# Kernel optimization log

Hardware: AMD Instinct MI355X
Metric: run time of the kernel (lower is better)

Reference implementation:

```python
import jax, jax.numpy as jnp
import numpy as np

H, D, K, FF = 4, 256, 1024, 1024  # n_head, d_model, key_feature_dim, dim_feedforward
L, B = 2048, 4                    # pixels, batch


def setup_inputs() -> dict:
    key = jax.random.key(0)
    ks = jax.random.split(key, 12)
    def g(k, shape, s=0.02):
        return jax.random.normal(k, shape, jnp.float32) * s
    return dict(
        src=jax.random.normal(ks[0], (L, B, D), jnp.float32),
        WK=g(ks[1], (H, K, D), (2.0 / K) ** 0.5),
        WQ=g(ks[2], (H, K, D), (2.0 / K) ** 0.5),
        WV=g(ks[3], (H, D, D), (2.0 / D) ** 0.5),
        TC=g(ks[4], (H, D, D)),
        ENw1=g(ks[5], (H, FF, D)), ENb1=jnp.zeros((H, FF), jnp.float32),
        ENw2=g(ks[6], (H, D, FF)), ENb2=jnp.zeros((H, D), jnp.float32),
        ENg=jnp.ones((H, D), jnp.float32), ENbeta=jnp.zeros((H, D), jnp.float32),
        Wout=g(ks[7], (D, H * D)),
        L1w=g(ks[8], (FF, D)), L1b=jnp.zeros((FF,), jnp.float32),
        L2w=g(ks[9], (D, FF)), L2b=jnp.zeros((D,), jnp.float32),
        N1g=jnp.ones((D,), jnp.float32), N1b=jnp.zeros((D,), jnp.float32),
        N2g=jnp.ones((D,), jnp.float32), N2b=jnp.zeros((D,), jnp.float32),
    )


def _ln(x, g, b, eps=1e-5):
    m = jnp.mean(x, -1, keepdims=True)
    v = jnp.mean((x - m) ** 2, -1, keepdims=True)
    return (x - m) * jax.lax.rsqrt(v + eps) * g + b


def _l2n(x, eps=1e-12):
    n = jnp.sqrt(jnp.sum(x * x, -1, keepdims=True))
    return x / jnp.maximum(n, eps)


def reference(src, WK, WQ, WV, TC, ENw1, ENb1, ENw2, ENb2, ENg, ENbeta,
              Wout, L1w, L1b, L2w, L2b, N1g, N1b, N2g, N2b):
    # --- RMA: per-head RelationUnit, vectorized over head axis h ---
    wq = _l2n(jnp.einsum('lbd,hkd->hlbk', src, WQ))   # (H,L,B,K), L2-normed
    wk = _l2n(jnp.einsum('lbd,hkd->hlbk', src, WK))
    wv = jnp.einsum('lbd,hed->hlbe', src, WV)         # (H,L,B,D)
    dot = jnp.einsum('hlbk,hmbk->hblm', wq, wk)       # (H,B,Lq,Lk)
    aff = jax.nn.softmax(dot, axis=-1)                 # softmax over keys (temp=1)
    aff = aff / (1e-9 + jnp.sum(aff, axis=2, keepdims=True))  # renorm over QUERY dim (torch dim=1)
    out = jnp.einsum('hblm,hmbe->hlbe', aff, wv)       # (H,L,B,D)
    ru = jax.nn.relu(jnp.einsum('hlbe,hfe->hlbf', src[None] - out, TC))
    # per-head extra TransNonlinear: residual MLP + layernorm
    hid = jax.nn.relu(jnp.einsum('hlbd,hfd->hlbf', ru, ENw1) + ENb1[:, None, None, :])
    s2 = jnp.einsum('hlbf,hdf->hlbd', hid, ENw2) + ENb2[:, None, None, :]
    tn = _ln(ru + s2, ENg[:, None, None, :], ENbeta[:, None, None, :])  # (H,L,B,D)
    concat = jnp.transpose(tn, (1, 2, 0, 3)).reshape(L, B, H * D)
    attn = concat @ Wout.T                              # (L,B,D)
    # --- encoder layer: residual + LN + FFN + LN (dropout = eval identity) ---
    x = _ln(src + attn, N1g, N1b)
    ff = jax.nn.relu(x @ L1w.T + L1b) @ L2w.T + L2b
    return _ln(x + ff, N2g, N2b)
```

## Files before the change

### kernel.cpp

```cpp
#include <hip/hip_runtime.h>
#include <hip/hip_bf16.h>

typedef __hip_bfloat16 bf16;
typedef short s16x8 __attribute__((ext_vector_type(8)));
typedef float f32x4 __attribute__((ext_vector_type(4)));

#define HN 4
#define DM 256
#define KF 1024
#define FFD 1024
#define LL 2048
#define BB 4
#define NN (LL * BB)
#define HD (HN * DM)

__device__ __forceinline__ float b2f(unsigned short u) {
    unsigned v = ((unsigned)u) << 16; float f; __builtin_memcpy(&f, &v, 4); return f;
}
__device__ __forceinline__ unsigned short f2b(float f) {
    bf16 b = (bf16)f; unsigned short u; __builtin_memcpy(&u, &b, 2); return u;
}

__device__ __forceinline__ float waveReduceSum(float v) {
    for (int o = 32; o; o >>= 1) v += __shfl_down(v, o, 64);
    return v;
}
__device__ __forceinline__ float waveReduceMax(float v) {
    for (int o = 32; o; o >>= 1) v = fmaxf(v, __shfl_down(v, o, 64));
    return v;
}
__device__ __forceinline__ float blockReduceSum(float v) {
    __shared__ float sh[4];
    v = waveReduceSum(v);
    __syncthreads();
    if ((threadIdx.x & 63) == 0) sh[threadIdx.x >> 6] = v;
    __syncthreads();
    return sh[0] + sh[1] + sh[2] + sh[3];
}
__device__ __forceinline__ float blockReduceMax(float v) {
    __shared__ float sh[4];
    v = waveReduceMax(v);
    __syncthreads();
    if ((threadIdx.x & 63) == 0) sh[threadIdx.x >> 6] = v;
    __syncthreads();
    return fmaxf(fmaxf(sh[0], sh[1]), fmaxf(sh[2], sh[3]));
}

__global__ void sentinel_kernel(float* out, float val) {
    if (threadIdx.x == 0 && blockIdx.x == 0) out[0] = val;
}

__device__ __forceinline__ void gll16(const void* g, void* l) {
#if defined(__HIP_DEVICE_COMPILE__)
    __builtin_amdgcn_global_load_lds(
        (const __attribute__((address_space(1))) unsigned int*)g,
        (__attribute__((address_space(3))) unsigned int*)l, 16, 0, 0);
#endif
}

#define VMC(n) asm volatile("s_waitcnt vmcnt(" #n ")" ::: "memory")
#define LGKM0() asm volatile("s_waitcnt lgkmcnt(0)" ::: "memory")

__global__ __launch_bounds__(512) void gemm256(
    const bf16* __restrict__ A, int lda, long sA,
    const bf16* __restrict__ Bv, int ldb, long sB,
    void* __restrict__ C, int cF32, int ldc, long sC,
    int Kc,
    const float* __restrict__ bias, long sBias,
    const void* __restrict__ aux, int auxType, int ldaux, long sAux,
    float accSign, int relu)
{
    const int z = blockIdx.z;
    const bf16* Ah = A + (long)z * sA;
    const bf16* Bh = Bv + (long)z * sB;
    float* Cf = (float*)C + (long)z * sC;
    bf16*  Ch = (bf16*)C + (long)z * sC;
    const float* biasp = bias ? (bias + (long)z * sBias) : nullptr;
    const float* auxf = (auxType == 1) ? ((const float*)aux + (long)z * sAux) : nullptr;
    const bf16*  auxh = (auxType == 2) ? ((const bf16*)aux + (long)z * sAux) : nullptr;

    __shared__ __align__(16) bf16 As[2][256 * 64];
    __shared__ __align__(16) bf16 Bs[2][256 * 64];

    const int tid  = threadIdx.x;
    const int lane = tid & 63;
    const int wid  = __builtin_amdgcn_readfirstlane(tid >> 6);
    const int wm   = wid >> 2;
    const int wn   = wid & 3;
    const int lrow = lane & 15;
    const int quad = lane >> 4;
    const int m0 = blockIdx.x * 256;
    const int n0 = blockIdx.y * 256;

    const int srow8  = wid * 8 + (lane >> 3);
    const int scolsw = ((lane & 7) * 8) ^ ((srow8 & 7) << 3);
    const bf16* Aorg = Ah + (long)m0 * lda;
    const bf16* Borg = Bh + (long)n0 * ldb;

    const int colx = (lane & 7) << 3;
    const int kc0 = (quad * 8) ^ colx;
    const int kc1 = (32 + quad * 8) ^ colx;

    f32x4 acc[8][4] = {};
    s16x8 afr[4][2], bfr[4][2];

    const int nk = Kc >> 6;

    auto stg = [&](const bf16* org, int ld, bf16* lds, int k0, int h) {
#pragma unroll
        for (int j = 0; j < 2; j++) {
            int rl = h * 128 + j * 64 + srow8;
            gll16((const void*)(org + (long)rl * ld + k0 + scolsw),
                  (void*)(lds + (h * 128 + j * 64 + wid * 8) * 64));
        }
    };

    stg(Aorg, lda, As[0], 0, 0); stg(Aorg, lda, As[0], 0, 1);
    stg(Borg, ldb, Bs[0], 0, 0); stg(Borg, ldb, Bs[0], 0, 1);
    if (nk > 1) {
        stg(Aorg, lda, As[1], 64, 0); stg(Aorg, lda, As[1], 64, 1);
        stg(Borg, ldb, Bs[1], 64, 0); stg(Borg, ldb, Bs[1], 64, 1);
        VMC(8);
    } else {
        VMC(0);
    }
    __builtin_amdgcn_s_barrier();

    for (int t = 0; t < nk; ++t) {
        const int s = t & 1;
        const bf16* Acur = As[s];
        const bf16* Bcur = Bs[s];
        bf16* Anxt = As[s ^ 1];
        bf16* Bslot = Bs[s];
        const bool stA = (t >= 1) && (t + 1 < nk);
        const bool stB = (t + 2 < nk);

#pragma unroll
        for (int mi = 0; mi < 4; mi++) {
            int r = (wm * 128 + mi * 16 + lrow) * 64;
            afr[mi][0] = *(const s16x8*)&Acur[r + kc0];
            afr[mi][1] = *(const s16x8*)&Acur[r + kc1];
        }
#pragma unroll
        for (int ni = 0; ni < 2; ni++) {
            int r = (wn * 64 + ni * 16 + lrow) * 64;
            bfr[ni][0] = *(const s16x8*)&Bcur[r + kc0];
            bfr[ni][1] = *(const s16x8*)&Bcur[r + kc1];
        }
        if (stA) stg(Aorg, lda, Anxt, (t + 1) << 6, 0);
        __builtin_amdgcn_s_barrier();
        LGKM0();
        __builtin_amdgcn_s_setprio(1);
#pragma unroll
        for (int mi = 0; mi < 4; mi++)
#pragma unroll
            for (int ni = 0; ni < 2; ni++)
#pragma unroll
                for (int ks = 0; ks < 2; ks++)
                    acc[mi][ni] = __builtin_amdgcn_mfma_f32_16x16x32_bf16(afr[mi][ks], bfr[ni][ks], acc[mi][ni], 0, 0, 0);
        __builtin_amdgcn_s_setprio(0);
        __builtin_amdgcn_s_barrier();

#pragma unroll
        for (int ni = 0; ni < 2; ni++) {
            int r = (wn * 64 + (2 + ni) * 16 + lrow) * 64;
            bfr[2 + ni][0] = *(const s16x8*)&Bcur[r + kc0];
            bfr[2 + ni][1] = *(const s16x8*)&Bcur[r + kc1];
        }
        if (stA) stg(Aorg, lda, Anxt, (t + 1) << 6, 1);
        __builtin_amdgcn_s_barrier();
        LGKM0();
        __builtin_amdgcn_s_setprio(1);
#pragma unroll
        for (int mi = 0; mi < 4; mi++)
#pragma unroll
            for (int ni = 0; ni < 2; ni++)
#pragma unroll
                for (int ks = 0; ks < 2; ks++)
                    acc[mi][2 + ni] = __builtin_amdgcn_mfma_f32_16x16x32_bf16(afr[mi][ks], bfr[2 + ni][ks], acc[mi][2 + ni], 0, 0, 0);
        __builtin_amdgcn_s_setprio(0);
        __builtin_amdgcn_s_barrier();

#pragma unroll
        for (int mi = 0; mi < 4; mi++) {
            int r = (wm * 128 + 64 + mi * 16 + lrow) * 64;
            afr[mi][0] = *(const s16x8*)&Acur[r + kc0];
            afr[mi][1] = *(const s16x8*)&Acur[r + kc1];
        }
        if (stB) stg(Borg, ldb, Bslot, (t + 2) << 6, 0);
        __builtin_amdgcn_s_barrier();
        LGKM0();
        __builtin_amdgcn_s_setprio(1);
#pragma unroll
        for (int mi = 0; mi < 4; mi++)
#pragma unroll
            for (int ni = 0; ni < 2; ni++)
#pragma unroll
                for (int ks = 0; ks < 2; ks++)
                    acc[4 + mi][ni] = __builtin_amdgcn_mfma_f32_16x16x32_bf16(afr[mi][ks], bfr[ni][ks], acc[4 + mi][ni], 0, 0, 0);
        __builtin_amdgcn_s_setprio(0);
        __builtin_amdgcn_s_barrier();

        if (stB) stg(Borg, ldb, Bslot, (t + 2) << 6, 1);
        __builtin_amdgcn_s_barrier();
        __builtin_amdgcn_s_setprio(1);
#pragma unroll
        for (int mi = 0; mi < 4; mi++)
#pragma unroll
            for (int ni = 0; ni < 2; ni++)
#pragma unroll
                for (int ks = 0; ks < 2; ks++)
                    acc[4 + mi][2 + ni] = __builtin_amdgcn_mfma_f32_16x16x32_bf16(afr[mi][ks], bfr[2 + ni][ks], acc[4 + mi][2 + ni], 0, 0, 0);
        __builtin_amdgcn_s_setprio(0);
        if (stB) { VMC(4); } else { VMC(0); }
        __builtin_amdgcn_s_barrier();
    }

#pragma unroll
    for (int mi = 0; mi < 8; mi++) {
#pragma unroll
        for (int ni = 0; ni < 4; ni++) {
            int col = n0 + wn * 64 + ni * 16 + lrow;
            float bvl = biasp ? biasp[col] : 0.0f;
#pragma unroll
            for (int i = 0; i < 4; i++) {
                int row = m0 + wm * 128 + mi * 16 + quad * 4 + i;
                float v = accSign * acc[mi][ni][i] + bvl;
                if (auxType == 1) v += auxf[(long)row * ldaux + col];
                else if (auxType == 2) v += (float)auxh[(long)row * ldaux + col];
                if (relu) v = fmaxf(v, 0.0f);
                if (cF32) Cf[(long)row * ldc + col] = v;
                else Ch[(long)row * ldc + col] = (bf16)v;
            }
        }
    }
}

template<int BN>
__global__ __launch_bounds__(256) void gemm_nt(
    const void* __restrict__ A, int aF32, int lda, long sA,
    const void* __restrict__ Bv, int bF32, int ldb, long sB,
    void* __restrict__ C, int cF32, int ldc, long sC,
    int Kc,
    const float* __restrict__ bias, long sBias,
    const void* __restrict__ aux, int auxType, int ldaux, long sAux,
    float accSign, int relu)
{
    constexpr int NI = BN / 32;
    constexpr int WN = BN / 2;
    const int z = blockIdx.z;
    const float* Af = (const float*)A + (long)z * sA;
    const bf16*  Ah = (const bf16*)A + (long)z * sA;
    const float* Bf = (const float*)Bv + (long)z * sB;
    const bf16*  Bh = (const bf16*)Bv + (long)z * sB;
    float* Cf = (float*)C + (long)z * sC;
    bf16*  Ch = (bf16*)C + (long)z * sC;
    const float* biasp = bias ? (bias + (long)z * sBias) : nullptr;
    const float* auxf = (auxType == 1) ? ((const float*)aux + (long)z * sAux) : nullptr;
    const bf16*  auxh = (auxType == 2) ? ((const bf16*)aux + (long)z * sAux) : nullptr;

    __shared__ __align__(16) bf16 As[2][128 * 32];
    __shared__ __align__(16) bf16 Bs[2][BN * 32];

    const int tid = threadIdx.x;
    const int lane = tid & 63;
    const int wv = __builtin_amdgcn_readfirstlane(tid >> 6);
    const int wm = (tid >> 6) & 1;
    const int wn = (tid >> 6) >> 1;
    const int lrow = lane & 15;
    const int quad = lane >> 4;
    const int m0 = blockIdx.x * 128;
    const int n0 = blockIdx.y * BN;
    const int srow = tid >> 1;
    const int scol = (tid & 1) * 16;
    const int drow = wv * 16 + (lane >> 2);
    const int dcol = (lane & 3) * 8;

    f32x4 acc[4][NI] = {};

    if (!aF32 && !bF32) {
        const int nk = Kc >> 5;
        auto stage = [&](int k0, int buf) {
            const bf16* a0 = Ah + (long)(m0 + drow) * lda + k0 + dcol;
            gll16((const void*)a0, (void*)&As[buf][wv * 512]);
            gll16((const void*)(a0 + (long)lda * 64), (void*)&As[buf][2048 + wv * 512]);
            const bf16* b0 = Bh + (long)(n0 + drow) * ldb + k0 + dcol;
            gll16((const void*)b0, (void*)&Bs[buf][wv * 512]);
            if (BN == 128)
                gll16((const void*)(b0 + (long)ldb * 64), (void*)&Bs[buf][2048 + wv * 512]);
        };
        stage(0, 0);
        __syncthreads();
        int cur = 0;
        for (int t = 0; t < nk; ++t) {
            if (t + 1 < nk) stage((t + 1) << 5, cur ^ 1);
            s16x8 af[4], bfg[NI];
#pragma unroll
            for (int mi = 0; mi < 4; mi++)
                af[mi] = *(const s16x8*)&As[cur][(wm * 64 + mi * 16 + lrow) * 32 + quad * 8];
#pragma unroll
            for (int ni = 0; ni < NI; ni++)
                bfg[ni] = *(const s16x8*)&Bs[cur][(wn * WN + ni * 16 + lrow) * 32 + quad * 8];
#pragma unroll
            for (int mi = 0; mi < 4; mi++)
#pragma unroll
                for (int ni = 0; ni < NI; ni++)
                    acc[mi][ni] = __builtin_amdgcn_mfma_f32_16x16x32_bf16(af[mi], bfg[ni], acc[mi][ni], 0, 0, 0);
            __syncthreads();
            cur ^= 1;
        }
    } else {
        for (int k0 = 0; k0 < Kc; k0 += 32) {
            uint4 av0, av1, bv0, bv1;
            if (aF32) {
                const float* ag = Af + (long)(m0 + srow) * lda + k0 + scol;
                ushort t[16];
#pragma unroll
                for (int j = 0; j < 4; j++) {
                    float4 f = *(const float4*)(ag + 4 * j);
                    t[4*j] = f2b(f.x); t[4*j+1] = f2b(f.y); t[4*j+2] = f2b(f.z); t[4*j+3] = f2b(f.w);
                }
                av0 = *(const uint4*)&t[0]; av1 = *(const uint4*)&t[8];
            }
            if (bF32) {
                if (srow < BN) {
                    const float* bg = Bf + (long)(n0 + srow) * ldb + k0 + scol;
                    ushort t[16];
#pragma unroll
                    for (int j = 0; j < 4; j++) {
                        float4 f = *(const float4*)(bg + 4 * j);
                        t[4*j] = f2b(f.x); t[4*j+1] = f2b(f.y); t[4*j+2] = f2b(f.z); t[4*j+3] = f2b(f.w);
                    }
                    bv0 = *(const uint4*)&t[0]; bv1 = *(const uint4*)&t[8];
                }
            }
            __syncthreads();
            if (aF32) {
                *(uint4*)&As[0][srow * 32 + scol] = av0;
                *(uint4*)&As[0][srow * 32 + scol + 8] = av1;
            } else {
                gll16((const void*)(Ah + (long)(m0 + drow) * lda + k0 + dcol), (void*)&As[0][wv * 512]);
                gll16((const void*)(Ah + (long)(m0 + 64 + drow) * lda + k0 + dcol), (void*)&As[0][2048 + wv * 512]);
            }
            if (bF32) {
                if (srow < BN) {
                    *(uint4*)&Bs[0][srow * 32 + scol] = bv0;
                    *(uint4*)&Bs[0][srow * 32 + scol + 8] = bv1;
                }
            } else {
                gll16((const void*)(Bh + (long)(n0 + drow) * ldb + k0 + dcol), (void*)&Bs[0][wv * 512]);
                if (BN == 128)
                    gll16((const void*)(Bh + (long)(n0 + 64 + drow) * ldb + k0 + dcol), (void*)&Bs[0][2048 + wv * 512]);
            }
            __syncthreads();

            s16x8 af[4], bfg[NI];
#pragma unroll
            for (int mi = 0; mi < 4; mi++)
                af[mi] = *(const s16x8*)&As[0][(wm * 64 + mi * 16 + lrow) * 32 + quad * 8];
#pragma unroll
            for (int ni = 0; ni < NI; ni++)
                bfg[ni] = *(const s16x8*)&Bs[0][(wn * WN + ni * 16 + lrow) * 32 + quad * 8];
#pragma unroll
            for (int mi = 0; mi < 4; mi++)
#pragma unroll
                for (int ni = 0; ni < NI; ni++)
                    acc[mi][ni] = __builtin_amdgcn_mfma_f32_16x16x32_bf16(af[mi], bfg[ni], acc[mi][ni], 0, 0, 0);
        }
    }

#pragma unroll
    for (int mi = 0; mi < 4; mi++) {
#pragma unroll
        for (int ni = 0; ni < NI; ni++) {
            int col = n0 + wn * WN + ni * 16 + lrow;
            float bvl = biasp ? biasp[col] : 0.0f;
#pragma unroll
            for (int i = 0; i < 4; i++) {
                int row = m0 + wm * 64 + mi * 16 + quad * 4 + i;
                float v = accSign * acc[mi][ni][i] + bvl;
                if (auxType == 1) v += auxf[(long)row * ldaux + col];
                else if (auxType == 2) v += (float)auxh[(long)row * ldaux + col];
                if (relu) v = fmaxf(v, 0.0f);
                if (cF32) Cf[(long)row * ldc + col] = v;
                else Ch[(long)row * ldc + col] = (bf16)v;
            }
        }
    }
}

__global__ __launch_bounds__(256) void cvt4(const float* __restrict__ in, bf16* __restrict__ out, int n4) {
    int i = blockIdx.x * 256 + threadIdx.x;
    if (i < n4) {
        float4 f = ((const float4*)in)[i];
        ushort4 u; u.x = f2b(f.x); u.y = f2b(f.y); u.z = f2b(f.z); u.w = f2b(f.w);
        ((ushort4*)out)[i] = u;
    }
}

struct WCvt {
    const float* in[9];
    bf16* out[9];
    int n4[9];
};
__global__ __launch_bounds__(256) void cvt_weights(WCvt wc) {
    int t = blockIdx.y;
    int n4 = wc.n4[t];
    const float4* in = (const float4*)wc.in[t];
    ushort4* out = (ushort4*)wc.out[t];
    for (int i = blockIdx.x * 256 + threadIdx.x; i < n4; i += gridDim.x * 256) {
        float4 f = in[i];
        ushort4 u; u.x = f2b(f.x); u.y = f2b(f.y); u.z = f2b(f.z); u.w = f2b(f.w);
        out[i] = u;
    }
}

__global__ __launch_bounds__(256) void l2norm_rows(bf16* __restrict__ Q) {
    bf16* q = Q + (long)blockIdx.x * KF;
    ushort4 u = ((ushort4*)q)[threadIdx.x];
    float v0 = b2f(u.x), v1 = b2f(u.y), v2 = b2f(u.z), v3 = b2f(u.w);
    float ss = blockReduceSum(v0 * v0 + v1 * v1 + v2 * v2 + v3 * v3);
    float inv = 1.0f / fmaxf(sqrtf(ss), 1e-12f);
    u.x = f2b(v0 * inv); u.y = f2b(v1 * inv); u.z = f2b(v2 * inv); u.w = f2b(v3 * inv);
    ((ushort4*)q)[threadIdx.x] = u;
}

__global__ __launch_bounds__(256) void softmax_rows(bf16* __restrict__ P) {
    bf16* p = P + (long)blockIdx.x * LL;
    ushort4 a = ((ushort4*)p)[2 * threadIdx.x];
    ushort4 b = ((ushort4*)p)[2 * threadIdx.x + 1];
    float v[8] = {b2f(a.x), b2f(a.y), b2f(a.z), b2f(a.w), b2f(b.x), b2f(b.y), b2f(b.z), b2f(b.w)};
    float mx = -1e30f;
#pragma unroll
    for (int i = 0; i < 8; i++) mx = fmaxf(mx, v[i]);
    mx = blockReduceMax(mx);
    float s = 0.0f;
#pragma unroll
    for (int i = 0; i < 8; i++) { v[i] = __expf(v[i] - mx); s += v[i]; }
    s = blockReduceSum(s);
    float inv = 1.0f / s;
    a.x = f2b(v[0]*inv); a.y = f2b(v[1]*inv); a.z = f2b(v[2]*inv); a.w = f2b(v[3]*inv);
    b.x = f2b(v[4]*inv); b.y = f2b(v[5]*inv); b.z = f2b(v[6]*inv); b.w = f2b(v[7]*inv);
    ((ushort4*)p)[2 * threadIdx.x] = a;
    ((ushort4*)p)[2 * threadIdx.x + 1] = b;
}

__global__ __launch_bounds__(256) void zero_cs(float* __restrict__ cs) {
    cs[blockIdx.x * 256 + threadIdx.x] = 0.0f;
}

__global__ __launch_bounds__(256) void colsum2(const bf16* __restrict__ P, float* __restrict__ cs) {
    int col = blockIdx.x * 256 + threadIdx.x;
    int rc = blockIdx.y;
    int b = blockIdx.z;
    const bf16* p = P + (long)b * LL * LL + (long)rc * 128 * LL + col;
    float s = 0.0f;
#pragma unroll 4
    for (int r = 0; r < 128; r++) s += (float)p[(long)r * LL];
    atomicAdd(&cs[(long)b * LL + col], s);
}

__global__ __launch_bounds__(256) void scale_vt(bf16* __restrict__ vt, const float* __restrict__ cs) {
    int e = blockIdx.x, b = blockIdx.y;
    bf16* row = vt + ((long)b * DM + e) * LL;
    const float* c = cs + (long)b * LL;
#pragma unroll
    for (int i = 0; i < 8; i++) {
        int m = threadIdx.x + i * 256;
        row[m] = (bf16)((float)row[m] / (1e-9f + c[m]));
    }
}

__global__ __launch_bounds__(256) void ln_rows(const bf16* __restrict__ in, void* __restrict__ out,
                                               int outF32,
                                               const float* __restrict__ g, const float* __restrict__ b,
                                               const float* __restrict__ aux) {
    long base = (long)blockIdx.x * 256;
    float v = (float)in[base + threadIdx.x];
    if (aux) v += aux[base + threadIdx.x];
    float mean = blockReduceSum(v) * (1.0f / 256.0f);
    float d = v - mean;
    float var = blockReduceSum(d * d) * (1.0f / 256.0f);
    float o = d * rsqrtf(var + 1e-5f) * g[threadIdx.x] + b[threadIdx.x];
    if (outF32) ((float*)out)[base + threadIdx.x] = o;
    else ((bf16*)out)[base + threadIdx.x] = (bf16)o;
}

__global__ __launch_bounds__(256) void ln_cat(bf16* __restrict__ cat, const float* __restrict__ g,
                                              const float* __restrict__ bb) {
    long n = blockIdx.x;
    int h = blockIdx.y;
    bf16* x = cat + n * HD + (long)h * DM;
    float v = (float)x[threadIdx.x];
    float mean = blockReduceSum(v) * (1.0f / 256.0f);
    float d = v - mean;
    float var = blockReduceSum(d * d) * (1.0f / 256.0f);
    x[threadIdx.x] = (bf16)(d * rsqrtf(var + 1e-5f) * g[h * DM + threadIdx.x] + bb[h * DM + threadIdx.x]);
}

extern "C" void kernel_launch(void* const* d_in, const int* in_sizes, int n_in,
                              void* d_out, int out_size, void* d_ws, size_t ws_size,
                              hipStream_t stream) {
    const float* src  = (const float*)d_in[0];
    const float* WK   = (const float*)d_in[1];
    const float* WQ   = (const float*)d_in[2];
    const float* WV   = (const float*)d_in[3];
    const float* TC   = (const float*)d_in[4];
    const float* ENw1 = (const float*)d_in[5];
    const float* ENb1 = (const float*)d_in[6];
    const float* ENw2 = (const float*)d_in[7];
    const float* ENb2 = (const float*)d_in[8];
    const float* ENg  = (const float*)d_in[9];
    const float* ENbt = (const float*)d_in[10];
    const float* Wout = (const float*)d_in[11];
    const float* L1w  = (const float*)d_in[12];
    const float* L1b  = (const float*)d_in[13];
    const float* L2w  = (const float*)d_in[14];
    const float* L2b  = (const float*)d_in[15];
    const float* N1g  = (const float*)d_in[16];
    const float* N1b  = (const float*)d_in[17];
    const float* N2g  = (const float*)d_in[18];
    const float* N2b  = (const float*)d_in[19];

    const size_t COMPACT_FLOOR = 34700000;
    const size_t FAST_FLOOR  = 92307456;
    const size_t FASTW_FLOOR = 92307456 + 11010048;
    if (ws_size < COMPACT_FLOOR || out_size != NN * DM || n_in != 20) {
        float val;
        if (n_in != 20) val = 32768.0f + (float)n_in;
        else if (out_size != NN * DM) val = 49152.0f;
        else val = 16384.0f + 128.0f * (float)(unsigned)(ws_size >> 20);
        sentinel_kernel<<<1, 64, 0, stream>>>((float*)d_out, val);
        return;
    }

    char* w = (char*)d_ws;
    auto G = [&](const void* A, int aF, int lda, long sA,
                 const void* B, int bF, int ldb, long sB,
                 void* C, int cF, int ldc, long sC,
                 int M, int Nn, int Kc, int nb,
                 const float* bias, long sBias,
                 const void* aux, int auxT, int ldaux, long sAux,
                 float sgn, int relu) {
        gemm_nt<128><<<dim3(M / 128, Nn / 128, nb), dim3(256), 0, stream>>>(
            A, aF, lda, sA, B, bF, ldb, sB, C, cF, ldc, sC, Kc,
            bias, sBias, aux, auxT, ldaux, sAux, sgn, relu);
    };
    auto G64 = [&](const void* A, int aF, int lda, long sA,
                 const void* B, int bF, int ldb, long sB,
                 void* C, int cF, int ldc, long sC,
                 int M, int Nn, int Kc, int nb,
                 const float* bias, long sBias,
                 const void* aux, int auxT, int ldaux, long sAux,
                 float sgn, int relu) {
        gemm_nt<64><<<dim3(M / 128, Nn / 64, nb), dim3(256), 0, stream>>>(
            A, aF, lda, sA, B, bF, ldb, sB, C, cF, ldc, sC, Kc,
            bias, sBias, aux, auxT, ldaux, sAux, sgn, relu);
    };
    auto G2 = [&](const void* A, int lda, long sA,
                  const void* B, int ldb, long sB,
                  void* C, int cF, int ldc, long sC,
                  int M, int Nn, int Kc, int nb,
                  const float* bias, long sBias,
                  const void* aux, int auxT, int ldaux, long sAux,
                  float sgn, int relu) {
        gemm256<<<dim3(M / 256, Nn / 256, nb), dim3(512), 0, stream>>>(
            (const bf16*)A, lda, sA, (const bf16*)B, ldb, sB, C, cF, ldc, sC, Kc,
            bias, sBias, aux, auxT, ldaux, sAux, sgn, relu);
    };

    if (ws_size >= FAST_FLOOR) {
        bf16*  Sb  = (bf16*)(w + 0);
        bf16*  Q   = (bf16*)(w + 4194304);
        bf16*  K   = (bf16*)(w + 20971520);
        bf16*  Vt  = (bf16*)(w + 37748736);
        bf16*  P   = (bf16*)(w + 41943040);
        bf16*  Su  = (bf16*)(w + 75497472);
        float* Cs  = (float*)(w + 92274688);
        bf16* Ru = Q; bf16* Hid = K; bf16* Cat = P;
        bf16* Attn = Vt; bf16* Xln = Su; bf16* Ffh = Q; bf16* Yp = Vt;

        const int haveWb = (ws_size >= FASTW_FLOOR) ? 1 : 0;
        char* wb = w + 92307456;
        bf16* WKb   = (bf16*)(wb + 0);
        bf16* WQb   = (bf16*)(wb + 2097152);
        bf16* WVb   = (bf16*)(wb + 4194304);
        bf16* TCb   = (bf16*)(wb + 4718592);
        bf16* ENw1b = (bf16*)(wb + 5242880);
        bf16* ENw2b = (bf16*)(wb + 7340032);
        bf16* Woutb = (bf16*)(wb + 9437184);
        bf16* L1wb  = (bf16*)(wb + 9961472);
        bf16* L2wb  = (bf16*)(wb + 10485760);
        if (haveWb) {
            WCvt wc;
            wc.in[0] = WK;   wc.out[0] = WKb;   wc.n4[0] = 262144;
            wc.in[1] = WQ;   wc.out[1] = WQb;   wc.n4[1] = 262144;
            wc.in[2] = WV;   wc.out[2] = WVb;   wc.n4[2] = 65536;
            wc.in[3] = TC;   wc.out[3] = TCb;   wc.n4[3] = 65536;
            wc.in[4] = ENw1; wc.out[4] = ENw1b; wc.n4[4] = 262144;
            wc.in[5] = ENw2; wc.out[5] = ENw2b; wc.n4[5] = 262144;
            wc.in[6] = Wout; wc.out[6] = Woutb; wc.n4[6] = 65536;
            wc.in[7] = L1w;  wc.out[7] = L1wb;  wc.n4[7] = 65536;
            wc.in[8] = L2w;  wc.out[8] = L2wb;  wc.n4[8] = 65536;
            cvt_weights<<<dim3(256, 9), 256, 0, stream>>>(wc);
        }
        const int wF = haveWb ? 0 : 1;
        auto WP = [&](const void* f32p, const void* b16p, long off) {
            return haveWb ? (const void*)((const bf16*)b16p + off)
                          : (const void*)((const float*)f32p + off);
        };

        cvt4<<<2048, 256, 0, stream>>>(src, Sb, NN * DM / 4);

        for (int h = 0; h < HN; h++) {
            G(Sb, 0, DM, 0, WP(WQ, WQb, (long)h * KF * DM), wF, DM, 0, Q, 0, KF, 0,
              NN, KF, DM, 1, nullptr, 0, nullptr, 0, 0, 0, 1.0f, 0);
            G(Sb, 0, DM, 0, WP(WK, WKb, (long)h * KF * DM), wF, DM, 0, K, 0, KF, 0,
              NN, KF, DM, 1, nullptr, 0, nullptr, 0, 0, 0, 1.0f, 0);
            G64(WP(WV, WVb, (long)h * DM * DM), wF, DM, 0, Sb, 0, BB * DM, DM,
              Vt, 0, LL, (long)DM * LL,
              DM, LL, DM, BB, nullptr, 0, nullptr, 0, 0, 0, 1.0f, 0);
            l2norm_rows<<<NN, 256, 0, stream>>>(Q);
            l2norm_rows<<<NN, 256, 0, stream>>>(K);
            G2(Q, BB * KF, KF, K, BB * KF, KF, P, 0, LL, (long)LL * LL,
               LL, LL, KF, BB, nullptr, 0, nullptr, 0, 0, 0, 1.0f, 0);
            softmax_rows<<<BB * LL, 256, 0, stream>>>(P);
            zero_cs<<<BB * LL / 256, 256, 0, stream>>>(Cs);
            colsum2<<<dim3(LL / 256, 16, BB), 256, 0, stream>>>(P, Cs);
            scale_vt<<<dim3(DM, BB), 256, 0, stream>>>(Vt, Cs);
            G64(P, 0, LL, (long)LL * LL, Vt, 0, LL, (long)DM * LL,
              Su + (long)h * NN * DM, 0, BB * DM, DM,
              LL, DM, LL, BB, nullptr, 0, Sb, 2, BB * DM, DM, -1.0f, 0);
        }
        G(Su, 0, DM, (long)NN * DM, WP(TC, TCb, 0), wF, DM, (long)DM * DM,
          Ru, 0, DM, (long)NN * DM,
          NN, DM, DM, HN, nullptr, 0, nullptr, 0, 0, 0, 1.0f, 1);
        for (int h = 0; h < HN; h++) {
            G(Ru + (long)h * NN * DM, 0, DM, 0, WP(ENw1, ENw1b, (long)h * FFD * DM), wF, DM, 0,
              Hid, 0, FFD, 0, NN, FFD, DM, 1, ENb1 + (long)h * FFD, 0, nullptr, 0, 0, 0, 1.0f, 1);
            G64(Hid, 0, FFD, 0, WP(ENw2, ENw2b, (long)h * DM * FFD), wF, FFD, 0,
              Cat + (long)h * DM, 0, HD, 0, NN, DM, FFD, 1,
              ENb2 + (long)h * DM, 0, Ru + (long)h * NN * DM, 2, DM, 0, 1.0f, 0);
        }
        ln_cat<<<dim3(NN, HN), 256, 0, stream>>>(Cat, ENg, ENbt);
        G64(Cat, 0, HD, 0, WP(Wout, Woutb, 0), wF, HD, 0, Attn, 0, DM, 0,
          NN, DM, HD, 1, nullptr, 0, nullptr, 0, 0, 0, 1.0f, 0);
        ln_rows<<<NN, 256, 0, stream>>>(Attn, Xln, 0, N1g, N1b, src);
        G(Xln, 0, DM, 0, WP(L1w, L1wb, 0), wF, DM, 0, Ffh, 0, FFD, 0,
          NN, FFD, DM, 1, L1b, 0, nullptr, 0, 0, 0, 1.0f, 1);
        G64(Ffh, 0, FFD, 0, WP(L2w, L2wb, 0), wF, FFD, 0, Yp, 0, DM, 0,
          NN, DM, FFD, 1, L2b, 0, Xln, 2, DM, 0, 1.0f, 0);
        ln_rows<<<NN, 256, 0, stream>>>(Yp, (float*)d_out, 1, N2g, N2b, nullptr);
    } else {
        bf16*  S0 = (bf16*)(w + 0);
        bf16*  S1 = (bf16*)(w + 16777216);
        bf16*  S2 = (bf16*)(w + 20971520);
        bf16*  S3 = (bf16*)(w + 25165824);
        bf16*  S4 = (bf16*)(w + 26214400);
        bf16*  S5 = (bf16*)(w + 30408704);
        float* Cs = (float*)(w + 34603008);

        for (int h = 0; h < HN; h++) {
            for (int b = 0; b < BB; b++) {
                G(src + b * DM, 1, BB * DM, 0, WQ + (long)h * KF * DM, 1, DM, 0,
                  S1, 0, KF, 0, LL, KF, DM, 1, nullptr, 0, nullptr, 0, 0, 0, 1.0f, 0);
                G(src + b * DM, 1, BB * DM, 0, WK + (long)h * KF * DM, 1, DM, 0,
                  S2, 0, KF, 0, LL, KF, DM, 1, nullptr, 0, nullptr, 0, 0, 0, 1.0f, 0);
                G(WV + (long)h * DM * DM, 1, DM, 0, src + b * DM, 1, BB * DM, 0,
                  S3, 0, LL, 0, DM, LL, DM, 1, nullptr, 0, nullptr, 0, 0, 0, 1.0f, 0);
                l2norm_rows<<<LL, 256, 0, stream>>>(S1);
                l2norm_rows<<<LL, 256, 0, stream>>>(S2);
                G(S1, 0, KF, 0, S2, 0, KF, 0, S0, 0, LL, 0,
                  LL, LL, KF, 1, nullptr, 0, nullptr, 0, 0, 0, 1.0f, 0);
                softmax_rows<<<LL, 256, 0, stream>>>(S0);
                zero_cs<<<LL / 256, 256, 0, stream>>>(Cs);
                colsum2<<<dim3(LL / 256, 16, 1), 256, 0, stream>>>(S0, Cs);
                scale_vt<<<dim3(DM, 1), 256, 0, stream>>>(S3, Cs);
                G(S0, 0, LL, 0, S3, 0, LL, 0, S4 + b * DM, 0, BB * DM, 0,
                  LL, DM, LL, 1, nullptr, 0, src + b * DM, 1, BB * DM, 0, -1.0f, 0);
            }
            G(S4, 0, DM, 0, TC + (long)h * DM * DM, 1, DM, 0, S1, 0, DM, 0,
              NN, DM, DM, 1, nullptr, 0, nullptr, 0, 0, 0, 1.0f, 1);
            G(S1, 0, DM, 0, ENw1 + (long)h * FFD * DM, 1, DM, 0, S0, 0, FFD, 0,
              NN, FFD, DM, 1, ENb1 + (long)h * FFD, 0, nullptr, 0, 0, 0, 1.0f, 1);
            G(S0, 0, FFD, 0, ENw2 + (long)h * DM * FFD, 1, FFD, 0, S2, 0, DM, 0,
              NN, DM, FFD, 1, ENb2 + (long)h * DM, 0, S1, 2, DM, 0, 1.0f, 0);
            ln_rows<<<NN, 256, 0, stream>>>(S2, S2, 0, ENg + (long)h * DM, ENbt + (long)h * DM, nullptr);
            G(S2, 0, DM, 0, Wout + (long)h * DM, 1, HD, 0, S5, 0, DM, 0,
              NN, DM, DM, 1, nullptr, 0, (h == 0) ? nullptr : (const void*)S5,
              (h == 0) ? 0 : 2, DM, 0, 1.0f, 0);
        }
        ln_rows<<<NN, 256, 0, stream>>>(S5, S1, 0, N1g, N1b, src);
        G(S1, 0, DM, 0, L1w, 1, DM, 0, S0, 0, FFD, 0,
          NN, FFD, DM, 1, L1b, 0, nullptr, 0, 0, 0, 1.0f, 1);
        G(S0, 0, FFD, 0, L2w, 1, FFD, 0, S2, 0, DM, 0,
          NN, DM, FFD, 1, L2b, 0, S1, 2, DM, 0, 1.0f, 0);
        ln_rows<<<NN, 256, 0, stream>>>(S2, (float*)d_out, 1, N2g, N2b, nullptr);
    }
}
```

Baseline: 1.081 ms.

## Fuse Q/K projections into one GEMM and triple-buffer the bf16 GEMM mainloop

Packs the per-head WQ and WK bf16 weights together so each head's Q and K projections run as one wide GEMM (N=2048) writing an interleaved QK buffer. The two L2-norm launches become one 2D launch, and the affinity GEMM reads Q and K from the interleaved buffer with stride 2048. The bf16 GEMM mainloop moves from double to triple buffering, using explicit vmcnt waits plus s_barrier so loads run two stages ahead. This cuts launch count and improves load/compute overlap, at the cost of more LDS per block, which may lower occupancy.

```diff
diff --git a/kernel.cpp b/kernel.cpp
--- a/kernel.cpp
+++ b/kernel.cpp
@@ -259,8 +259,8 @@
     const float* auxf = (auxType == 1) ? ((const float*)aux + (long)z * sAux) : nullptr;
     const bf16*  auxh = (auxType == 2) ? ((const bf16*)aux + (long)z * sAux) : nullptr;
 
-    __shared__ __align__(16) bf16 As[2][128 * 32];
-    __shared__ __align__(16) bf16 Bs[2][BN * 32];
+    __shared__ __align__(16) bf16 As[3][128 * 32];
+    __shared__ __align__(16) bf16 Bs[3][BN * 32];
 
     const int tid = threadIdx.x;
     const int lane = tid & 63;
@@ -280,7 +280,9 @@
 
     if (!aF32 && !bF32) {
         const int nk = Kc >> 5;
-        auto stage = [&](int k0, int buf) {
+        auto stage = [&](int t) {
+            const int buf = t % 3;
+            const int k0 = t << 5;
             const bf16* a0 = Ah + (long)(m0 + drow) * lda + k0 + dcol;
             gll16((const void*)a0, (void*)&As[buf][wv * 512]);
             gll16((const void*)(a0 + (long)lda * 64), (void*)&As[buf][2048 + wv * 512]);
@@ -289,11 +291,17 @@
             if (BN == 128)
                 gll16((const void*)(b0 + (long)ldb * 64), (void*)&Bs[buf][2048 + wv * 512]);
         };
-        stage(0, 0);
-        __syncthreads();
-        int cur = 0;
+        stage(0);
+        if (nk > 1) {
+            stage(1);
+            if constexpr (BN == 128) { VMC(4); } else { VMC(3); }
+        } else {
+            VMC(0);
+        }
+        __builtin_amdgcn_s_barrier();
         for (int t = 0; t < nk; ++t) {
-            if (t + 1 < nk) stage((t + 1) << 5, cur ^ 1);
+            const int cur = t % 3;
+            if (t + 2 < nk) stage(t + 2);
             s16x8 af[4], bfg[NI];
 #pragma unroll
             for (int mi = 0; mi < 4; mi++)
@@ -306,8 +314,12 @@
 #pragma unroll
                 for (int ni = 0; ni < NI; ni++)
                     acc[mi][ni] = __builtin_amdgcn_mfma_f32_16x16x32_bf16(af[mi], bfg[ni], acc[mi][ni], 0, 0, 0);
-            __syncthreads();
-            cur ^= 1;
+            if (t + 2 < nk) {
+                if constexpr (BN == 128) { VMC(4); } else { VMC(3); }
+            } else {
+                VMC(0);
+            }
+            __builtin_amdgcn_s_barrier();
         }
     } else {
         for (int k0 = 0; k0 < Kc; k0 += 32) {
@@ -399,9 +411,9 @@
 }
 
 struct WCvt {
-    const float* in[9];
-    bf16* out[9];
-    int n4[9];
+    const float* in[16];
+    bf16* out[16];
+    int n4[16];
 };
 __global__ __launch_bounds__(256) void cvt_weights(WCvt wc) {
     int t = blockIdx.y;
@@ -417,6 +429,16 @@
 
 __global__ __launch_bounds__(256) void l2norm_rows(bf16* __restrict__ Q) {
     bf16* q = Q + (long)blockIdx.x * KF;
+    ushort4 u = ((ushort4*)q)[threadIdx.x];
+    float v0 = b2f(u.x), v1 = b2f(u.y), v2 = b2f(u.z), v3 = b2f(u.w);
+    float ss = blockReduceSum(v0 * v0 + v1 * v1 + v2 * v2 + v3 * v3);
+    float inv = 1.0f / fmaxf(sqrtf(ss), 1e-12f);
+    u.x = f2b(v0 * inv); u.y = f2b(v1 * inv); u.z = f2b(v2 * inv); u.w = f2b(v3 * inv);
+    ((ushort4*)q)[threadIdx.x] = u;
+}
+
+__global__ __launch_bounds__(256) void l2norm2(bf16* __restrict__ QK) {
+    bf16* q = QK + (long)blockIdx.x * 2048 + (long)blockIdx.y * 1024;
     ushort4 u = ((ushort4*)q)[threadIdx.x];
     float v0 = b2f(u.x), v1 = b2f(u.y), v2 = b2f(u.z), v3 = b2f(u.w);
     float ss = blockReduceSum(v0 * v0 + v1 * v1 + v2 * v2 + v3 * v3);
@@ -577,13 +599,13 @@
         bf16*  P   = (bf16*)(w + 41943040);
         bf16*  Su  = (bf16*)(w + 75497472);
         float* Cs  = (float*)(w + 92274688);
+        bf16* QK = Q;
         bf16* Ru = Q; bf16* Hid = K; bf16* Cat = P;
         bf16* Attn = Vt; bf16* Xln = Su; bf16* Ffh = Q; bf16* Yp = Vt;
 
         const int haveWb = (ws_size >= FASTW_FLOOR) ? 1 : 0;
         char* wb = w + 92307456;
-        bf16* WKb   = (bf16*)(wb + 0);
-        bf16* WQb   = (bf16*)(wb + 2097152);
+        bf16* WQKb  = (bf16*)(wb + 0);
         bf16* WVb   = (bf16*)(wb + 4194304);
         bf16* TCb   = (bf16*)(wb + 4718592);
         bf16* ENw1b = (bf16*)(wb + 5242880);
@@ -593,16 +615,18 @@
         bf16* L2wb  = (bf16*)(wb + 10485760);
         if (haveWb) {
             WCvt wc;
-            wc.in[0] = WK;   wc.out[0] = WKb;   wc.n4[0] = 262144;
-            wc.in[1] = WQ;   wc.out[1] = WQb;   wc.n4[1] = 262144;
-            wc.in[2] = WV;   wc.out[2] = WVb;   wc.n4[2] = 65536;
-            wc.in[3] = TC;   wc.out[3] = TCb;   wc.n4[3] = 65536;
-            wc.in[4] = ENw1; wc.out[4] = ENw1b; wc.n4[4] = 262144;
-            wc.in[5] = ENw2; wc.out[5] = ENw2b; wc.n4[5] = 262144;
-            wc.in[6] = Wout; wc.out[6] = Woutb; wc.n4[6] = 65536;
-            wc.in[7] = L1w;  wc.out[7] = L1wb;  wc.n4[7] = 65536;
-            wc.in[8] = L2w;  wc.out[8] = L2wb;  wc.n4[8] = 65536;
-            cvt_weights<<<dim3(256, 9), 256, 0, stream>>>(wc);
+            for (int h = 0; h < HN; h++) {
+                wc.in[2*h]   = WQ + (long)h * KF * DM; wc.out[2*h]   = WQKb + (long)h * 2048 * DM;            wc.n4[2*h]   = 65536;
+                wc.in[2*h+1] = WK + (long)h * KF * DM; wc.out[2*h+1] = WQKb + (long)h * 2048 * DM + KF * DM;  wc.n4[2*h+1] = 65536;
+            }
+            wc.in[8]  = WV;   wc.out[8]  = WVb;   wc.n4[8]  = 65536;
+            wc.in[9]  = TC;   wc.out[9]  = TCb;   wc.n4[9]  = 65536;
+            wc.in[10] = ENw1; wc.out[10] = ENw1b; wc.n4[10] = 262144;
+            wc.in[11] = ENw2; wc.out[11] = ENw2b; wc.n4[11] = 262144;
+            wc.in[12] = Wout; wc.out[12] = Woutb; wc.n4[12] = 65536;
+            wc.in[13] = L1w;  wc.out[13] = L1wb;  wc.n4[13] = 65536;
+            wc.in[14] = L2w;  wc.out[14] = L2wb;  wc.n4[14] = 65536;
+            cvt_weights<<<dim3(256, 15), 256, 0, stream>>>(wc);
         }
         const int wF = haveWb ? 0 : 1;
         auto WP = [&](const void* f32p, const void* b16p, long off) {
@@ -613,16 +637,20 @@
         cvt4<<<2048, 256, 0, stream>>>(src, Sb, NN * DM / 4);
 
         for (int h = 0; h < HN; h++) {
-            G(Sb, 0, DM, 0, WP(WQ, WQb, (long)h * KF * DM), wF, DM, 0, Q, 0, KF, 0,
-              NN, KF, DM, 1, nullptr, 0, nullptr, 0, 0, 0, 1.0f, 0);
-            G(Sb, 0, DM, 0, WP(WK, WKb, (long)h * KF * DM), wF, DM, 0, K, 0, KF, 0,
-              NN, KF, DM, 1, nullptr, 0, nullptr, 0, 0, 0, 1.0f, 0);
+            if (haveWb) {
+                G2(Sb, DM, 0, WQKb + (long)h * 2048 * DM, DM, 0, QK, 0, 2048, 0,
+                   NN, 2048, DM, 1, nullptr, 0, nullptr, 0, 0, 0, 1.0f, 0);
+            } else {
+                G(Sb, 0, DM, 0, WQ + (long)h * KF * DM, 1, DM, 0, QK, 0, 2048, 0,
+                  NN, KF, DM, 1, nullptr, 0, nullptr, 0, 0, 0, 1.0f, 0);
+                G(Sb, 0, DM, 0, WK + (long)h * KF * DM, 1, DM, 0, QK + KF, 0, 2048, 0,
+                  NN, KF, DM, 1, nullptr, 0, nullptr, 0, 0, 0, 1.0f, 0);
+            }
             G64(WP(WV, WVb, (long)h * DM * DM), wF, DM, 0, Sb, 0, BB * DM, DM,
               Vt, 0, LL, (long)DM * LL,
               DM, LL, DM, BB, nullptr, 0, nullptr, 0, 0, 0, 1.0f, 0);
-            l2norm_rows<<<NN, 256, 0, stream>>>(Q);
-            l2norm_rows<<<NN, 256, 0, stream>>>(K);
-            G2(Q, BB * KF, KF, K, BB * KF, KF, P, 0, LL, (long)LL * LL,
+            l2norm2<<<dim3(NN, 2), 256, 0, stream>>>(QK);
+            G2(QK, 4 * 2048, 2048, QK + 1024, 4 * 2048, 2048, P, 0, LL, (long)LL * LL,
                LL, LL, KF, BB, nullptr, 0, nullptr, 0, 0, 0, 1.0f, 0);
             softmax_rows<<<BB * LL, 256, 0, stream>>>(P);
             zero_cs<<<BB * LL / 256, 256, 0, stream>>>(Cs);
```

Result: no change. 1.061 ms (-1.9%).
